# Kernel tuning notes

Hardware: AMD Instinct MI355X
Metric: run time of the kernel (lower is better)

Reference implementation:

```python
import jax, jax.numpy as jnp
import numpy as np
import math

B, LQ, LK, D, H = 4, 1024, 1024, 1024, 16
DK = D // H
SCALE = 1.0 / math.sqrt(DK)
NEG_INF = -1.0e9


def setup_inputs() -> dict:
    key = jax.random.key(0)
    ks = jax.random.split(key, 18)
    w = lambda k: (jax.random.normal(k, (D, D), dtype=jnp.float32) * 0.02)
    b = lambda k: (jax.random.normal(k, (D,), dtype=jnp.float32) * 0.02)
    mask = jax.random.randint(ks[4], (B, 1, LK), 0, 2).astype(jnp.int32)
    mask = mask.at[..., 0].set(1)  # ensure at least one valid key per row
    return {
        "query": jax.random.normal(ks[0], (B, LQ, D), dtype=jnp.float32),
        "key": jax.random.normal(ks[1], (B, LK, D), dtype=jnp.float32),
        "value": jax.random.normal(ks[2], (B, LK, D), dtype=jnp.float32),
        "weak_rela": jax.random.normal(ks[3], (B, LK, D), dtype=jnp.float32),
        "mask": mask,
        "Wq": w(ks[5]), "bq": b(ks[6]),
        "Wk": w(ks[7]), "bk": b(ks[8]),
        "Wv": w(ks[9]), "bv": b(ks[10]),
        "Wrk": w(ks[11]), "brk": b(ks[12]),
        "Wrv": w(ks[13]), "brv": b(ks[14]),
        "Wo": w(ks[15]), "bo": b(ks[16]),
    }


def _proj(x, W, bias):
    # x: [B, L, D] -> [B, H, L, DK]; torch Linear: y = x @ W.T + b
    y = x @ W.T + bias
    Bn, L, _ = y.shape
    return y.reshape(Bn, L, H, DK).transpose(0, 2, 1, 3)


def reference(query, key, value, weak_rela, mask,
              Wq, bq, Wk, bk, Wv, bv, Wrk, brk, Wrv, brv, Wo, bo):
    q = _proj(query, Wq, bq)        # [B,H,LQ,DK]
    k = _proj(key, Wk, bk)          # [B,H,LK,DK]
    v = _proj(value, Wv, bv)        # [B,H,LK,DK]
    rk = _proj(weak_rela, Wrk, brk) # [B,H,LK,DK]
    rv = _proj(weak_rela, Wrv, brv) # [B,H,LK,DK]

    qk = jnp.einsum('bhqd,bhkd->bhqk', q, k) * SCALE
    qr = jnp.einsum('bhqd,bhkd->bhqk', q, rk) * SCALE

    m = (mask[:, None, :, :] == 0)  # [B,1,1,LK] broadcast over heads/queries
    qk = jnp.where(m, NEG_INF, qk)
    qr = jnp.where(m, NEG_INF, qr)

    p_vis = jax.nn.softmax(qk, axis=-1)
    p_rel = jax.nn.softmax(qr, axis=-1)

    x = (jnp.einsum('bhqk,bhkd->bhqd', p_vis, v)
         + jnp.einsum('bhqk,bhkd->bhqd', p_rel, rv))  # [B,H,LQ,DK]
    x = x.transpose(0, 2, 1, 3).reshape(query.shape[0], -1, H * DK)
    return x @ Wo.T + bo
```

## Files before the change

kernel.cpp:

```cpp
#include <hip/hip_runtime.h>
#include <stdint.h>

#define NB 4
#define NH 16
#define DKH 64
#define DMODEL 1024
#define SEQ 1024
#define SCALE 0.125f
#define NEG_INF -1.0e9f
#define K2E 0.18033688011112042f

typedef __bf16 bf16_t;
typedef __bf16 bf16x8 __attribute__((ext_vector_type(8)));
typedef __bf16 bf16x4v __attribute__((ext_vector_type(4)));
typedef float f32x4 __attribute__((ext_vector_type(4)));

typedef const uint32_t __attribute__((address_space(1)))* gas_ptr;
typedef uint32_t __attribute__((address_space(3)))* las_ptr;

__device__ __forceinline__ void gload_lds16(const void* g, void* l) {
  __builtin_amdgcn_global_load_lds((gas_ptr)g, (las_ptr)l, 16, 0, 0);
}


__global__ void cvt_multi(const float* __restrict__ i0, const float* __restrict__ i1,
                          const float* __restrict__ i2, const float* __restrict__ i3,
                          const float* __restrict__ i4, const float* __restrict__ i5,
                          bf16_t* o0, bf16_t* o1, bf16_t* o2, bf16_t* o3, bf16_t* o4, bf16_t* o5,
                          int n) {
  const int t = blockIdx.y;
  const float* in = (t == 0) ? i0 : (t == 1) ? i1 : (t == 2) ? i2 : (t == 3) ? i3 : (t == 4) ? i4 : i5;
  bf16_t* out = (t == 0) ? o0 : (t == 1) ? o1 : (t == 2) ? o2 : (t == 3) ? o3 : (t == 4) ? o4 : o5;
  const int idx = (blockIdx.x * 256 + threadIdx.x) * 4;
  if (idx >= n) return;
  const float4 v = *(const float4*)(in + idx);
  bf16x4v p;
  p[0] = (bf16_t)v.x; p[1] = (bf16_t)v.y; p[2] = (bf16_t)v.z; p[3] = (bf16_t)v.w;
  *(bf16x4v*)(out + idx) = p;
}

#define NXE ((size_t)NB * SEQ * DMODEL)
#define NWE ((size_t)DMODEL * DMODEL)

template<int MODE>
__device__ __forceinline__ void gemm128_body(
    const bf16_t* __restrict__ A, const bf16_t* __restrict__ W,
    const float* __restrict__ bias, void* __restrict__ outp,
    int m0, int n0, bf16_t* As, bf16_t* Bs) {
  const int tid = threadIdx.x;
  const int lane = tid & 63;
  const int w = tid >> 6;
  const int wm = w >> 1, wn = w & 1;
  const int g = lane >> 4, c = lane & 15;
  const int lrow = lane >> 3;
  const int lcol = ((lane & 7) * 8) ^ ((lane >> 3) << 3);
  const int sc = (c & 7) << 3;

  f32x4 acc[4][4] = {};

  for (int kt = 0; kt < DMODEL; kt += 64) {
#pragma unroll
    for (int p = 0; p < 4; ++p) {
      const int row = w * 32 + p * 8;
      gload_lds16(A + (size_t)(m0 + row + lrow) * DMODEL + kt + lcol, &As[row * 64]);
      gload_lds16(W + (size_t)(n0 + row + lrow) * DMODEL + kt + lcol, &Bs[row * 64]);
    }
    __syncthreads();
    bf16x8 af[4][2], bfr[4][2];
#pragma unroll
    for (int i = 0; i < 4; ++i)
#pragma unroll
      for (int kk = 0; kk < 2; ++kk) {
        af[i][kk]  = *(const bf16x8*)&As[(wm * 64 + i * 16 + c) * 64 + ((kk * 32 + g * 8) ^ sc)];
        bfr[i][kk] = *(const bf16x8*)&Bs[(wn * 64 + i * 16 + c) * 64 + ((kk * 32 + g * 8) ^ sc)];
      }
#pragma unroll
    for (int i = 0; i < 4; ++i)
#pragma unroll
      for (int j = 0; j < 4; ++j) {
        acc[i][j] = __builtin_amdgcn_mfma_f32_16x16x32_bf16(af[i][0], bfr[j][0], acc[i][j], 0, 0, 0);
        acc[i][j] = __builtin_amdgcn_mfma_f32_16x16x32_bf16(af[i][1], bfr[j][1], acc[i][j], 0, 0, 0);
      }
    __syncthreads();
  }

  float bv4[4];
#pragma unroll
  for (int j = 0; j < 4; ++j) bv4[j] = bias[n0 + wn * 64 + j * 16 + c];

#pragma unroll
  for (int i = 0; i < 4; ++i) {
    const int mrow = m0 + wm * 64 + i * 16 + g * 4;
    const int b_ = mrow >> 10, l_ = mrow & 1023;
#pragma unroll
    for (int j = 0; j < 4; ++j) {
      const int n = n0 + wn * 64 + j * 16 + c;
      if (MODE == 2) {
        float* o = (float*)outp;
#pragma unroll
        for (int r = 0; r < 4; ++r)
          o[(size_t)(mrow + r) * DMODEL + n] = acc[i][j][r] + bv4[j];
      } else if (MODE == 0) {
        bf16_t* o = (bf16_t*)outp;
        const int h_ = n >> 6, dk_ = n & 63;
#pragma unroll
        for (int r = 0; r < 4; ++r)
          o[((size_t)(b_ * NH + h_) * SEQ + l_ + r) * DKH + dk_] =
              (bf16_t)(acc[i][j][r] + bv4[j]);
      } else {
        bf16_t* o = (bf16_t*)outp;
        const int h_ = n >> 6, dk_ = n & 63;
        bf16x4v pk;
#pragma unroll
        for (int r = 0; r < 4; ++r) pk[r] = (bf16_t)(acc[i][j][r] + bv4[j]);
        *(bf16x4v*)&o[((size_t)(b_ * NH + h_) * DKH + dk_) * SEQ + l_] = pk;
      }
    }
  }
}

__global__ void __launch_bounds__(256, 2)
proj_gemm(const bf16_t* __restrict__ Xbase, const bf16_t* __restrict__ Wbase,
          bf16_t* __restrict__ Obase,
          const float* __restrict__ b0, const float* __restrict__ b1,
          const float* __restrict__ b2, const float* __restrict__ b3,
          const float* __restrict__ b4) {
  __shared__ bf16_t As[128 * 64];
  __shared__ bf16_t Bs[128 * 64];
  const int bid = blockIdx.x;
  const int lid = (bid & 7) * 160 + (bid >> 3);
  const int seg = lid >> 8;
  const int rr = lid & 255;
  const int m0 = (rr >> 3) * 128, n0 = (rr & 7) * 128;

  const bf16_t* A = Xbase + (size_t)((seg < 3) ? seg : 3) * NXE;
  const bf16_t* W = Wbase + (size_t)seg * NWE;
  const int ooff = (seg == 0) ? 0 : (seg == 1) ? 1 : (seg == 2) ? 3 : (seg == 3) ? 2 : 4;
  bf16_t* out = Obase + (size_t)ooff * NXE;
  const float* bias = (seg == 0) ? b0 : (seg == 1) ? b1 : (seg == 2) ? b2 : (seg == 3) ? b3 : b4;

  if (seg == 2 || seg == 4) gemm128_body<1>(A, W, bias, out, m0, n0, As, Bs);
  else                      gemm128_body<0>(A, W, bias, out, m0, n0, As, Bs);
}

__global__ void __launch_bounds__(256, 2)
out_gemm(const bf16_t* __restrict__ A, const bf16_t* __restrict__ W,
         const float* __restrict__ bias, float* __restrict__ out) {
  __shared__ bf16_t As[128 * 64];
  __shared__ bf16_t Bs[128 * 64];
  const int bid = blockIdx.x;
  const int lid = (bid & 7) * 32 + (bid >> 3);
  const int m0 = (lid >> 3) * 128, n0 = (lid & 7) * 128;
  gemm128_body<2>(A, W, bias, out, m0, n0, As, Bs);
}

__global__ void __launch_bounds__(256, 2)
attn_kernel(const bf16_t* __restrict__ q, const bf16_t* __restrict__ k,
            const bf16_t* __restrict__ rk, const bf16_t* __restrict__ vT,
            const bf16_t* __restrict__ rvT, const int* __restrict__ mask,
            bf16_t* __restrict__ x) {
  extern __shared__ __align__(256) bf16_t smem[];
  bf16_t* Ks  = smem;
  bf16_t* RKs = Ks  + 64 * 64;
  bf16_t* Vs  = RKs + 64 * 64;
  bf16_t* RVs = Vs  + 64 * 64;
  bf16_t* Pbase = RVs + 64 * 64;
  float* Mb = (float*)(Pbase + 8 * 2048);

  const int tid = threadIdx.x;
  const int lane = tid & 63;
  const int w = tid >> 6;
  const int g = lane >> 4, c = lane & 15;
  const int sc = (c & 7) << 3;
  const int bid = blockIdx.x;
  const int lid = (bid & 7) * 64 + (bid >> 3);
  const int qt = lid & 7;
  const int bh = lid >> 3;
  const int b = bh >> 4, h = bh & 15;
  const int q0 = qt * 128;

  const bf16_t* qp = q + (size_t)bh * SEQ * DKH;
  const bf16_t* kp = k + (size_t)bh * SEQ * DKH;
  const bf16_t* rkp = rk + (size_t)bh * SEQ * DKH;
  const bf16_t* vp = vT + (size_t)bh * DKH * SEQ;
  const bf16_t* rvp = rvT + (size_t)bh * DKH * SEQ;
  const int* mp = mask + b * SEQ;
  const int lrow = lane >> 3;
  const int lcol = ((lane & 7) * 8) ^ ((lane >> 3) << 3);

  bf16_t* Pwv = Pbase + w * 2048;
  bf16_t* Pwr = Pbase + (4 + w) * 2048;

#pragma unroll
  for (int i = 0; i < 4; ++i) {
    const int idx = i * 256 + tid;
    Mb[idx] = (mp[idx] == 0) ? NEG_INF : 0.0f;
  }

  bf16x8 qf[2][2];
#pragma unroll
  for (int i = 0; i < 2; ++i)
#pragma unroll
    for (int kk = 0; kk < 2; ++kk)
      qf[i][kk] = *(const bf16x8*)(qp + (size_t)(q0 + w * 32 + i * 16 + c) * DKH + kk * 32 + g * 8);

  f32x4 ov[2][4] = {}, orl[2][4] = {};
  float mv[2] = {NEG_INF, NEG_INF}, mr[2] = {NEG_INF, NEG_INF};
  float lv[2] = {0.f, 0.f}, lr[2] = {0.f, 0.f};

  auto qk_sm = [&](const bf16_t* Kt, bf16_t* Pb, const f32x4 (&mb)[4],
                   float (&m_s)[2], float (&l_s)[2], f32x4 (&o_s)[2][4]) {
    f32x4 s[2][4];
    {
      bf16x8 kfr[4][2];
#pragma unroll
      for (int f = 0; f < 4; ++f) {
        kfr[f][0] = *(const bf16x8*)&Kt[(f * 16 + c) * 64 + ((g * 8) ^ sc)];
        kfr[f][1] = *(const bf16x8*)&Kt[(f * 16 + c) * 64 + ((32 + g * 8) ^ sc)];
      }
#pragma unroll
      for (int i = 0; i < 2; ++i)
#pragma unroll
        for (int f = 0; f < 4; ++f) {
          f32x4 a = {0.f, 0.f, 0.f, 0.f};
          a = __builtin_amdgcn_mfma_f32_16x16x32_bf16(kfr[f][0], qf[i][0], a, 0, 0, 0);
          a = __builtin_amdgcn_mfma_f32_16x16x32_bf16(kfr[f][1], qf[i][1], a, 0, 0, 0);
          s[i][f] = a;
        }
    }

#pragma unroll
    for (int i = 0; i < 2; ++i)
#pragma unroll
      for (int f = 0; f < 4; ++f)
#pragma unroll
        for (int r = 0; r < 4; ++r)
          s[i][f][r] = s[i][f][r] * K2E + mb[f][r];

#pragma unroll
    for (int i = 0; i < 2; ++i) {
      float tm = fmaxf(fmaxf(s[i][0][0], s[i][0][1]), fmaxf(s[i][0][2], s[i][0][3]));
#pragma unroll
      for (int f = 1; f < 4; ++f)
        tm = fmaxf(tm, fmaxf(fmaxf(s[i][f][0], s[i][f][1]), fmaxf(s[i][f][2], s[i][f][3])));
      tm = fmaxf(tm, __shfl_xor(tm, 16));
      tm = fmaxf(tm, __shfl_xor(tm, 32));
      if (!__all(tm <= m_s[i] + 8.0f)) {
        const float mnew = fmaxf(m_s[i], tm);
        const float sf = __builtin_amdgcn_exp2f(m_s[i] - mnew);
        m_s[i] = mnew;
        l_s[i] *= sf;
#pragma unroll
        for (int jd = 0; jd < 4; ++jd)
#pragma unroll
          for (int r = 0; r < 4; ++r) o_s[i][jd][r] *= sf;
      }
      float pf = 0.f;
#pragma unroll
      for (int f = 0; f < 4; ++f) {
        bf16x4v pk;
#pragma unroll
        for (int r = 0; r < 4; ++r) {
          const float p = __builtin_amdgcn_exp2f(s[i][f][r] - m_s[i]);
          pf += p;
          pk[r] = (bf16_t)p;
        }
        *(bf16x4v*)&Pb[i * 1024 + c * 64 + ((f * 16 + g * 4) ^ sc)] = pk;
      }
      l_s[i] += pf;
    }
  };

  auto pv = [&](const bf16_t* Vt, const bf16_t* Pb, f32x4 (&o_s)[2][4]) {
    bf16x8 pa[2][2];
#pragma unroll
    for (int i = 0; i < 2; ++i) {
      pa[i][0] = *(const bf16x8*)&Pb[i * 1024 + c * 64 + ((g * 8) ^ sc)];
      pa[i][1] = *(const bf16x8*)&Pb[i * 1024 + c * 64 + ((32 + g * 8) ^ sc)];
    }
#pragma unroll
    for (int jd = 0; jd < 4; ++jd) {
      const bf16x8 v0 = *(const bf16x8*)&Vt[(jd * 16 + c) * 64 + ((g * 8) ^ sc)];
      const bf16x8 v1 = *(const bf16x8*)&Vt[(jd * 16 + c) * 64 + ((32 + g * 8) ^ sc)];
#pragma unroll
      for (int i = 0; i < 2; ++i) {
        o_s[i][jd] = __builtin_amdgcn_mfma_f32_16x16x32_bf16(v0, pa[i][0], o_s[i][jd], 0, 0, 0);
        o_s[i][jd] = __builtin_amdgcn_mfma_f32_16x16x32_bf16(v1, pa[i][1], o_s[i][jd], 0, 0, 0);
      }
    }
  };

  for (int t = 0; t < 16; ++t) {
    const int kv0 = t * 64;
    if (t) __syncthreads();
#pragma unroll
    for (int p = 0; p < 2; ++p) {
      const int row = w * 16 + p * 8;
      gload_lds16(kp  + (size_t)(kv0 + row + lrow) * DKH + lcol, &Ks[row * 64]);
      gload_lds16(rkp + (size_t)(kv0 + row + lrow) * DKH + lcol, &RKs[row * 64]);
      gload_lds16(vp  + (size_t)(row + lrow) * SEQ + kv0 + lcol, &Vs[row * 64]);
      gload_lds16(rvp + (size_t)(row + lrow) * SEQ + kv0 + lcol, &RVs[row * 64]);
    }
    __syncthreads();

    f32x4 mb[4];
#pragma unroll
    for (int f = 0; f < 4; ++f)
      mb[f] = *(const f32x4*)&Mb[kv0 + f * 16 + g * 4];

    qk_sm(Ks,  Pwv, mb, mv, lv, ov);
    qk_sm(RKs, Pwr, mb, mr, lr, orl);
    __builtin_amdgcn_s_setprio(1);
    pv(Vs,  Pwv, ov);
    pv(RVs, Pwr, orl);
    __builtin_amdgcn_s_setprio(0);
  }

#pragma unroll
  for (int i = 0; i < 2; ++i) {
    lv[i] += __shfl_xor(lv[i], 16); lv[i] += __shfl_xor(lv[i], 32);
    lr[i] += __shfl_xor(lr[i], 16); lr[i] += __shfl_xor(lr[i], 32);
  }

  bf16_t* xb = x + (size_t)b * SEQ * DMODEL + (size_t)h * DKH;
#pragma unroll
  for (int i = 0; i < 2; ++i) {
    const float rlv = 1.0f / lv[i], rlr = 1.0f / lr[i];
    const int qrow = q0 + w * 32 + i * 16 + c;
#pragma unroll
    for (int jd = 0; jd < 4; ++jd) {
      bf16x4v pk;
#pragma unroll
      for (int r = 0; r < 4; ++r)
        pk[r] = (bf16_t)(ov[i][jd][r] * rlv + orl[i][jd][r] * rlr);
      *(bf16x4v*)&xb[(size_t)qrow * DMODEL + jd * 16 + g * 4] = pk;
    }
  }
}

extern "C" void kernel_launch(void* const* d_in, const int* in_sizes, int n_in,
                              void* d_out, int out_size, void* d_ws, size_t ws_size,
                              hipStream_t stream) {
  (void)in_sizes; (void)n_in; (void)out_size; (void)ws_size;
  const float* query = (const float*)d_in[0];
  const float* key_  = (const float*)d_in[1];
  const float* value = (const float*)d_in[2];
  const float* weak  = (const float*)d_in[3];
  const int*   mask  = (const int*)d_in[4];
  const float* Wq  = (const float*)d_in[5];  const float* bq  = (const float*)d_in[6];
  const float* Wk  = (const float*)d_in[7];  const float* bk  = (const float*)d_in[8];
  const float* Wv  = (const float*)d_in[9];  const float* bv  = (const float*)d_in[10];
  const float* Wrk = (const float*)d_in[11]; const float* brk = (const float*)d_in[12];
  const float* Wrv = (const float*)d_in[13]; const float* brv = (const float*)d_in[14];
  const float* Wo  = (const float*)d_in[15]; const float* bo  = (const float*)d_in[16];

  char* ws = (char*)d_ws;
  size_t off = 0;
  auto alloc = [&](size_t bytes) {
    void* p = ws + off;
    off += (bytes + 255) & ~(size_t)255;
    return p;
  };
  const size_t SZ_X = NXE * sizeof(bf16_t);
  const size_t SZ_W = NWE * sizeof(bf16_t);

  bf16_t* Xq = (bf16_t*)alloc(SZ_X);
  bf16_t* Xk = (bf16_t*)alloc(SZ_X);
  bf16_t* Xv = (bf16_t*)alloc(SZ_X);
  bf16_t* Xr = (bf16_t*)alloc(SZ_X);
  bf16_t* Wqb  = (bf16_t*)alloc(SZ_W);
  bf16_t* Wkb  = (bf16_t*)alloc(SZ_W);
  bf16_t* Wvb  = (bf16_t*)alloc(SZ_W);
  bf16_t* Wrkb = (bf16_t*)alloc(SZ_W);
  bf16_t* Wrvb = (bf16_t*)alloc(SZ_W);
  bf16_t* Wob  = (bf16_t*)alloc(SZ_W);
  bf16_t* qh   = (bf16_t*)alloc(SZ_X);
  bf16_t* kh   = (bf16_t*)alloc(SZ_X);
  bf16_t* rkh  = (bf16_t*)alloc(SZ_X);
  bf16_t* vTh  = (bf16_t*)alloc(SZ_X);
  bf16_t* rvTh = (bf16_t*)alloc(SZ_X);
  bf16_t* xh   = (bf16_t*)alloc(SZ_X);
  (void)Xk; (void)Xv; (void)Xr; (void)Wkb; (void)Wvb; (void)Wrkb; (void)Wrvb;
  (void)kh; (void)rkh; (void)vTh; (void)rvTh;

  cvt_multi<<<dim3(4096, 4), 256, 0, stream>>>(query, key_, value, weak, nullptr, nullptr,
                                               Xq, Xk, Xv, Xr, nullptr, nullptr,
                                               NB * SEQ * DMODEL);
  cvt_multi<<<dim3(1024, 6), 256, 0, stream>>>(Wq, Wk, Wv, Wrk, Wrv, Wo,
                                               Wqb, Wkb, Wvb, Wrkb, Wrvb, Wob,
                                               DMODEL * DMODEL);

  proj_gemm<<<dim3(1280), 256, 0, stream>>>(Xq, Wqb, qh, bq, bk, bv, brk, brv);

  attn_kernel<<<dim3(512), 256, 69632, stream>>>(qh, kh, rkh, vTh, rvTh, mask, xh);

  out_gemm<<<dim3(256), 256, 0, stream>>>(xh, Wob, bo, (float*)d_out);
}
```

Baseline: 165.0 us.

## Prefetch next K/V tile into registers to overlap loads with compute

Replaces the direct global-to-LDS loads in the attention loop with register staging. The next tile's K, RK, V and RV are loaded into registers before the current tile is computed, then written to LDS (with an XOR swizzle) between two barriers. This is meant to hide global memory latency behind the MFMA work. In exchange it uses more VGPRs, which can lower occupancy, and adds an extra barrier per iteration.

```diff
diff --git a/kernel.cpp b/kernel.cpp
--- a/kernel.cpp
+++ b/kernel.cpp
@@ -14,6 +14,7 @@
 typedef __bf16 bf16x8 __attribute__((ext_vector_type(8)));
 typedef __bf16 bf16x4v __attribute__((ext_vector_type(4)));
 typedef float f32x4 __attribute__((ext_vector_type(4)));
+typedef uint32_t u32x4 __attribute__((ext_vector_type(4)));
 
 typedef const uint32_t __attribute__((address_space(1)))* gas_ptr;
 typedef uint32_t __attribute__((address_space(3)))* las_ptr;
@@ -185,8 +186,10 @@
   const bf16_t* vp = vT + (size_t)bh * DKH * SEQ;
   const bf16_t* rvp = rvT + (size_t)bh * DKH * SEQ;
   const int* mp = mask + b * SEQ;
+
   const int lrow = lane >> 3;
-  const int lcol = ((lane & 7) * 8) ^ ((lane >> 3) << 3);
+  const int lcolL = (lane & 7) * 8;
+  const int wcol = lcolL ^ (((w * 16 + lrow) & 7) << 3);
 
   bf16_t* Pwv = Pbase + w * 2048;
   bf16_t* Pwr = Pbase + (4 + w) * 2048;
@@ -207,6 +210,29 @@
   f32x4 ov[2][4] = {}, orl[2][4] = {};
   float mv[2] = {NEG_INF, NEG_INF}, mr[2] = {NEG_INF, NEG_INF};
   float lv[2] = {0.f, 0.f}, lr[2] = {0.f, 0.f};
+
+  u32x4 st[4][2];
+
+  auto ldreg = [&](int kv0) {
+#pragma unroll
+    for (int p = 0; p < 2; ++p) {
+      const int row = w * 16 + p * 8 + lrow;
+      st[0][p] = *(const u32x4*)(kp  + (size_t)(kv0 + row) * DKH + lcolL);
+      st[1][p] = *(const u32x4*)(rkp + (size_t)(kv0 + row) * DKH + lcolL);
+      st[2][p] = *(const u32x4*)(vp  + (size_t)row * SEQ + kv0 + lcolL);
+      st[3][p] = *(const u32x4*)(rvp + (size_t)row * SEQ + kv0 + lcolL);
+    }
+  };
+  auto wrlds = [&]() {
+#pragma unroll
+    for (int p = 0; p < 2; ++p) {
+      const int row = w * 16 + p * 8 + lrow;
+      *(u32x4*)&Ks [row * 64 + wcol] = st[0][p];
+      *(u32x4*)&RKs[row * 64 + wcol] = st[1][p];
+      *(u32x4*)&Vs [row * 64 + wcol] = st[2][p];
+      *(u32x4*)&RVs[row * 64 + wcol] = st[3][p];
+    }
+  };
 
   auto qk_sm = [&](const bf16_t* Kt, bf16_t* Pb, const f32x4 (&mb)[4],
                    float (&m_s)[2], float (&l_s)[2], f32x4 (&o_s)[2][4]) {
@@ -290,18 +316,14 @@
     }
   };
 
+  ldreg(0);
+  wrlds();
+  __syncthreads();
+
   for (int t = 0; t < 16; ++t) {
     const int kv0 = t * 64;
-    if (t) __syncthreads();
-#pragma unroll
-    for (int p = 0; p < 2; ++p) {
-      const int row = w * 16 + p * 8;
-      gload_lds16(kp  + (size_t)(kv0 + row + lrow) * DKH + lcol, &Ks[row * 64]);
-      gload_lds16(rkp + (size_t)(kv0 + row + lrow) * DKH + lcol, &RKs[row * 64]);
-      gload_lds16(vp  + (size_t)(row + lrow) * SEQ + kv0 + lcol, &Vs[row * 64]);
-      gload_lds16(rvp + (size_t)(row + lrow) * SEQ + kv0 + lcol, &RVs[row * 64]);
-    }
-    __syncthreads();
+
+    if (t < 15) ldreg(kv0 + 64);
 
     f32x4 mb[4];
 #pragma unroll
@@ -314,6 +336,12 @@
     pv(Vs,  Pwv, ov);
     pv(RVs, Pwr, orl);
     __builtin_amdgcn_s_setprio(0);
+
+    if (t < 15) {
+      __syncthreads();
+      wrlds();
+      __syncthreads();
+    }
   }
 
 #pragma unroll
```

New measurement: 164.5 us. No clear change (-0.3%).
